# Kernel optimization log

Hardware: AMD Instinct MI355X
Metric: run time of the kernel (lower is better)

The kernel has to match this reference:

```python
import jax, jax.numpy as jnp
import numpy as np

K = 20        # num_neighbor
EPS = 1e-5    # BatchNorm eps


def setup_inputs() -> dict:
    key = jax.random.key(0)
    ks = jax.random.split(key, 3)
    B, C, N = 8, 64, 2048
    points = jax.random.normal(ks[0], (B, C, N), dtype=jnp.float32)
    # 1x1 conv weights (out_ch, in_ch); BN affine params
    W0 = jax.random.normal(ks[1], (64, 2 * C), dtype=jnp.float32) * 0.05
    W1 = jax.random.normal(ks[2], (64, 64), dtype=jnp.float32) * 0.05
    return {
        "points": points,
        "W0": W0, "gamma0": jnp.ones((64,), jnp.float32), "beta0": jnp.zeros((64,), jnp.float32),
        "W1": W1, "gamma1": jnp.ones((64,), jnp.float32), "beta1": jnp.zeros((64,), jnp.float32),
    }


def _knn_idx(points, k):
    # points: (B, C, N) -> indices of k nearest neighbors (B, N, k)
    inner = jnp.einsum('bcn,bcm->bnm', points, points)          # (B,N,N)
    sq = jnp.sum(points * points, axis=1)                        # (B,N)
    dist = sq[:, :, None] - 2.0 * inner + sq[:, None, :]         # squared L2
    _, idx = jax.lax.top_k(-dist, k)                             # (B,N,k)
    return idx


def _edge_features(points, idx):
    # points: (B,C,N), idx: (B,N,K) -> (B, 2C, N, K) = concat([x_i, x_j - x_i])
    B, C, N = points.shape
    neigh = jnp.take_along_axis(points[:, :, None, :],           # (B,C,1,N)
                                idx[:, None, :, :], axis=3)      # (B,C,N,K)
    center = jnp.broadcast_to(points[:, :, :, None], neigh.shape)
    return jnp.concatenate([center, neigh - center], axis=1)     # (B,2C,N,K)


def _conv_bn_relu(x, W, gamma, beta):
    # 1x1 conv (no bias) + BatchNorm2d (training-mode batch stats) + ReLU
    h = jnp.einsum('oi,bink->bonk', W, x)
    mean = jnp.mean(h, axis=(0, 2, 3), keepdims=True)
    var = jnp.var(h, axis=(0, 2, 3), keepdims=True)
    h = (h - mean) * jax.lax.rsqrt(var + EPS)
    h = h * gamma[None, :, None, None] + beta[None, :, None, None]
    return jax.nn.relu(h)


def reference(points, W0, gamma0, beta0, W1, gamma1, beta1):
    idx = _knn_idx(points, K)                  # (B,N,K)
    feat = _edge_features(points, idx)         # (B,2C,N,K)
    feat = _conv_bn_relu(feat, W0, gamma0, beta0)
    feat = _conv_bn_relu(feat, W1, gamma1, beta1)
    return jnp.max(feat, axis=3)               # (B, out_ch, N)
```

## Files before the change

### kernel.cpp

```cpp
#include <hip/hip_runtime.h>

#define NPTS 2048
#define NB 8
#define NC 64
#define KNN 20
#define NSLOT 16
#define NMERGE 28
#define EPS 1e-5f
#define MTOT 327680.0f

#define WS_U_BYTE    1024
#define WS_V_BYTE    4195328
#define WS_IDX_BYTE  8389632
#define WS_SQD_BYTE  9700352
#define WS_SQ32_BYTE 9831424
#define WS_HMIN_BYTE 9700352

__device__ __forceinline__ unsigned umax2(unsigned a, unsigned b) { return a > b ? a : b; }
__device__ __forceinline__ unsigned umin2(unsigned a, unsigned b) { return a < b ? a : b; }

__global__ __launch_bounds__(256) void k_prep(const float* __restrict__ pts,
                                              const float* __restrict__ W0,
                                              double* __restrict__ sqd,
                                              float* __restrict__ sq32,
                                              float* __restrict__ u,
                                              float* __restrict__ v) {
  const int b  = blockIdx.x >> 5;
  const int n0 = (blockIdx.x & 31) << 6;
  const int tid = threadIdx.x;
  __shared__ float WdT[64][64];
  __shared__ float WbT[64][64];
  __shared__ float xs[64][64];
  for (int i = tid; i < 4096; i += 256) {
    int o = i & 63, c = i >> 6;
    float wa = W0[o * 128 + c], wb = W0[o * 128 + 64 + c];
    WdT[c][o] = wa - wb;
    WbT[c][o] = wb;
  }
  {
    int pp = tid & 63, c0 = tid >> 6;
    for (int i = 0; i < 16; i++) {
      int c = c0 + 4 * i;
      xs[c][pp] = pts[(b * 64 + c) * NPTS + n0 + pp];
    }
  }
  __syncthreads();
  if (tid < 64) {
    double s = 0.0;
    for (int c = 0; c < 64; c++) { double x = (double)xs[c][tid]; s += x * x; }
    sqd[b * NPTS + n0 + tid] = s;
    sq32[b * NPTS + n0 + tid] = (float)s;
  }
  const int o = tid & 63, w = tid >> 6;
  float wd[64], wb[64];
#pragma unroll
  for (int c = 0; c < 64; c++) { wd[c] = WdT[c][o]; wb[c] = WbT[c][o]; }
  for (int i = 0; i < 16; i++) {
    int p = w + 4 * i;
    float ua = 0.f, va = 0.f;
#pragma unroll
    for (int c = 0; c < 64; c++) {
      float xc = xs[c][p];
      ua += wd[c] * xc;
      va += wb[c] * xc;
    }
    int gp = b * NPTS + n0 + p;
    u[gp * 64 + o] = ua;
    v[gp * 64 + o] = va;
  }
}

__global__ __launch_bounds__(64) void k_knn(const float* __restrict__ pts,
                                            const double* __restrict__ sqd,
                                            const float* __restrict__ sq32,
                                            int* __restrict__ idxout) {
  const int b  = blockIdx.x >> 9;
  const int n0 = (blockIdx.x & 511) << 2;
  const int lane = threadIdx.x;
  __shared__ __align__(16) float4 rows4[64];
  __shared__ __align__(16) float distS[1024];
  const float* pb = pts + b * 64 * NPTS;
  rows4[lane] = *(const float4*)(pb + lane * NPTS + n0);
  float sqr[4];
#pragma unroll
  for (int rr = 0; rr < 4; rr++) sqr[rr] = sq32[b * NPTS + n0 + rr];
  __syncthreads();

  unsigned slot[NSLOT];
#pragma unroll
  for (int j = 0; j < NSLOT; j++) slot[j] = 0xFFFFF800u | (unsigned)j;
  unsigned wmax = 0xFFFFF800u | (NSLOT - 1);
  const int r = lane >> 4, g = lane & 15;

  for (int t = 0; t < 8; t++) {
    const int mb = t * 256;
    float facc[16];
#pragma unroll
    for (int i = 0; i < 16; i++) facc[i] = 0.f;
    const float4 sqm = *(const float4*)(sq32 + b * NPTS + mb + 4 * lane);
#pragma unroll 8
    for (int c = 0; c < 64; c++) {
      float4 xm = *(const float4*)(pb + c * NPTS + mb + 4 * lane);
      float4 xr = rows4[c];
      facc[0]  += xr.x * xm.x; facc[1]  += xr.x * xm.y; facc[2]  += xr.x * xm.z; facc[3]  += xr.x * xm.w;
      facc[4]  += xr.y * xm.x; facc[5]  += xr.y * xm.y; facc[6]  += xr.y * xm.z; facc[7]  += xr.y * xm.w;
      facc[8]  += xr.z * xm.x; facc[9]  += xr.z * xm.y; facc[10] += xr.z * xm.z; facc[11] += xr.z * xm.w;
      facc[12] += xr.w * xm.x; facc[13] += xr.w * xm.y; facc[14] += xr.w * xm.z; facc[15] += xr.w * xm.w;
    }
#pragma unroll
    for (int rr = 0; rr < 4; rr++) {
      float4 dd;
      dd.x = sqr[rr] + sqm.x - 2.f * facc[rr * 4 + 0];
      dd.y = sqr[rr] + sqm.y - 2.f * facc[rr * 4 + 1];
      dd.z = sqr[rr] + sqm.z - 2.f * facc[rr * 4 + 2];
      dd.w = sqr[rr] + sqm.w - 2.f * facc[rr * 4 + 3];
      *(float4*)&distS[rr * 256 + (lane & 3) * 64 + (lane >> 2) * 4] = dd;
    }
    __syncthreads();
#pragma unroll
    for (int j4 = 0; j4 < 4; j4++) {
      float4 dv = *(const float4*)&distS[r * 256 + j4 * 64 + g * 4];
      float dq[4] = {dv.x, dv.y, dv.z, dv.w};
#pragma unroll
      for (int q = 0; q < 4; q++) {
        int m = mb + g * 16 + j4 * 4 + q;
        unsigned ub = __float_as_uint(dq[q]);
        ub ^= (ub >> 31) ? 0xFFFFFFFFu : 0x80000000u;
        unsigned key = (ub & 0xFFFFF800u) | (unsigned)m;
        if (key < wmax) {
#pragma unroll
          for (int j = 0; j < NSLOT; j++)
            slot[j] = (slot[j] == wmax) ? key : slot[j];
          unsigned t8[8];
#pragma unroll
          for (int j = 0; j < 8; j++) t8[j] = umax2(slot[2 * j], slot[2 * j + 1]);
          unsigned t4a = umax2(t8[0], t8[1]), t4b = umax2(t8[2], t8[3]);
          unsigned t4c = umax2(t8[4], t8[5]), t4d = umax2(t8[6], t8[7]);
          wmax = umax2(umax2(t4a, t4b), umax2(t4c, t4d));
        }
      }
    }
    __syncthreads();
  }

  unsigned mycand[2] = {0xFFFFFFFFu, 0xFFFFFFFFu};
  for (int p = 0; p < NMERGE; p++) {
    unsigned t8[8];
#pragma unroll
    for (int j = 0; j < 8; j++) t8[j] = umin2(slot[2 * j], slot[2 * j + 1]);
    unsigned t4a = umin2(t8[0], t8[1]), t4b = umin2(t8[2], t8[3]);
    unsigned t4c = umin2(t8[4], t8[5]), t4d = umin2(t8[6], t8[7]);
    unsigned gmin = umin2(umin2(t4a, t4b), umin2(t4c, t4d));
#pragma unroll
    for (int mk = 1; mk < 16; mk <<= 1) {
      unsigned o = __shfl_xor(gmin, mk, 16);
      gmin = umin2(gmin, o);
    }
#pragma unroll
    for (int j = 0; j < NSLOT; j++)
      if (slot[j] == gmin) slot[j] = 0xFFFFFFFFu;
    if ((p & 15) == g) mycand[p >> 4] = gmin;
  }

  const int nrow = n0 + r;
  const float* rowsF = (const float*)rows4;
  unsigned long long ekey[2];
#pragma unroll
  for (int s = 0; s < 2; s++) {
    ekey[s] = ~0ull;
    if (mycand[s] != 0xFFFFFFFFu) {
      const int m = (int)(mycand[s] & 2047u);
      const float* pc = pb + m;
      double a0 = 0.0, a1 = 0.0, a2 = 0.0, a3 = 0.0;
      for (int c = 0; c < 64; c += 4) {
        a0 += (double)rowsF[(c + 0) * 4 + r] * (double)pc[(c + 0) * NPTS];
        a1 += (double)rowsF[(c + 1) * 4 + r] * (double)pc[(c + 1) * NPTS];
        a2 += (double)rowsF[(c + 2) * 4 + r] * (double)pc[(c + 2) * NPTS];
        a3 += (double)rowsF[(c + 3) * 4 + r] * (double)pc[(c + 3) * NPTS];
      }
      double d = sqd[b * NPTS + nrow] + sqd[b * NPTS + m] - 2.0 * ((a0 + a1) + (a2 + a3));
      unsigned long long ub = (unsigned long long)__double_as_longlong(d);
      ub ^= (ub >> 63) ? 0xFFFFFFFFFFFFFFFFull : 0x8000000000000000ull;
      ekey[s] = (ub & ~2047ull) | (unsigned long long)(unsigned)m;
    }
  }

  const int row = b * NPTS + nrow;
  for (int p = 0; p < KNN; p++) {
    unsigned long long lmin = ekey[0] < ekey[1] ? ekey[0] : ekey[1];
#pragma unroll
    for (int mk = 1; mk < 16; mk <<= 1) {
      unsigned long long o = __shfl_xor(lmin, mk, 16);
      lmin = o < lmin ? o : lmin;
    }
    if (g == 0) idxout[row * KNN + p] = (int)(lmin & 2047ull);
    if (ekey[0] == lmin) ekey[0] = ~0ull;
    if (ekey[1] == lmin) ekey[1] = ~0ull;
  }
}

__global__ __launch_bounds__(256) void k_stats0(const float* __restrict__ u,
                                                const float* __restrict__ v,
                                                const int* __restrict__ idx,
                                                float* __restrict__ stats) {
  const int tid = threadIdx.x, o = tid & 63, w = tid >> 6;
  float s1 = 0.f, s2 = 0.f;
  const int r0 = blockIdx.x * 64;
  for (int i = 0; i < 16; i++) {
    int row = r0 + w + 4 * i;
    int b = row >> 11;
    float uo = u[row * 64 + o];
    const int* ip = idx + row * KNN;
    for (int k = 0; k < KNN; k++) {
      int j = ip[k];
      float h = uo + v[(b * NPTS + j) * 64 + o];
      s1 += h; s2 += h * h;
    }
  }
  __shared__ float red[2][256];
  red[0][tid] = s1; red[1][tid] = s2;
  __syncthreads();
  if (tid < 64) {
    float a  = red[0][tid] + red[0][tid + 64] + red[0][tid + 128] + red[0][tid + 192];
    float bb = red[1][tid] + red[1][tid + 64] + red[1][tid + 128] + red[1][tid + 192];
    atomicAdd(&stats[o], a);
    atomicAdd(&stats[64 + o], bb);
  }
}

__global__ __launch_bounds__(256) void k_mid(const float* __restrict__ u,
                                             const float* __restrict__ v,
                                             const int* __restrict__ idx,
                                             const float* __restrict__ W1,
                                             const float* __restrict__ g0,
                                             const float* __restrict__ b0,
                                             const float* __restrict__ stats0,
                                             float* __restrict__ stats1,
                                             float* __restrict__ hmax,
                                             float* __restrict__ hmin) {
  const int tid = threadIdx.x, o = tid & 63, w = tid >> 6;
  __shared__ float W1s[64][65];
  __shared__ float hbuf[4][4][64];
  for (int i = tid; i < 4096; i += 256) W1s[i >> 6][i & 63] = W1[i];
  __syncthreads();
  float mean = stats0[o] / MTOT;
  float var  = stats0[64 + o] / MTOT - mean * mean;
  float a0 = g0[o] * rsqrtf(var + EPS);
  float c0 = b0[o] - mean * a0;
  float w1r[64];
#pragma unroll
  for (int c = 0; c < 64; c++) w1r[c] = W1s[o][c];
  float s1 = 0.f, s2 = 0.f;
  const int r0 = blockIdx.x * 16 + w * 4;
  for (int rr = 0; rr < 4; rr++) {
    const int row = r0 + rr;
    const int b = row >> 11, n = row & 2047;
    const float uo = u[row * 64 + o];
    const int* ip = idx + row * KNN;
    float hmx = -1e30f, hmn = 1e30f;
    for (int kb = 0; kb < 5; kb++) {
#pragma unroll
      for (int kk = 0; kk < 4; kk++) {
        int j = ip[kb * 4 + kk];
        float h0 = uo + v[(b * NPTS + j) * 64 + o];
        hbuf[w][kk][o] = fmaxf(a0 * h0 + c0, 0.f);
      }
      __syncthreads();
#pragma unroll
      for (int kk = 0; kk < 4; kk++) {
        float h1 = 0.f;
#pragma unroll
        for (int c4 = 0; c4 < 16; c4++) {
          float4 hh = *(const float4*)&hbuf[w][kk][c4 * 4];
          h1 += w1r[c4 * 4 + 0] * hh.x + w1r[c4 * 4 + 1] * hh.y +
                w1r[c4 * 4 + 2] * hh.z + w1r[c4 * 4 + 3] * hh.w;
        }
        s1 += h1; s2 += h1 * h1;
        hmx = fmaxf(hmx, h1); hmn = fminf(hmn, h1);
      }
      __syncthreads();
    }
    hmax[(b * 64 + o) * NPTS + n] = hmx;
    hmin[(b * 64 + o) * NPTS + n] = hmn;
  }
  __shared__ float red[2][256];
  red[0][tid] = s1; red[1][tid] = s2;
  __syncthreads();
  if (tid < 64) {
    float a  = red[0][tid] + red[0][tid + 64] + red[0][tid + 128] + red[0][tid + 192];
    float bb = red[1][tid] + red[1][tid + 64] + red[1][tid + 128] + red[1][tid + 192];
    atomicAdd(&stats1[o], a);
    atomicAdd(&stats1[64 + o], bb);
  }
}

__global__ __launch_bounds__(256) void k_final(const float* __restrict__ hmaxO,
                                               const float* __restrict__ hmin,
                                               const float* __restrict__ stats1,
                                               const float* __restrict__ g1,
                                               const float* __restrict__ b1,
                                               float* __restrict__ out) {
  const int i = blockIdx.x * 256 + threadIdx.x;
  const int o = (i >> 11) & 63;
  float mean = stats1[o] / MTOT;
  float var  = stats1[64 + o] / MTOT - mean * mean;
  float a1 = g1[o] * rsqrtf(var + EPS);
  float c1 = b1[o] - mean * a1;
  float pick = (a1 >= 0.f) ? hmaxO[i] : hmin[i];
  out[i] = fmaxf(a1 * pick + c1, 0.f);
}

extern "C" void kernel_launch(void* const* d_in, const int* in_sizes, int n_in,
                              void* d_out, int out_size, void* d_ws, size_t ws_size,
                              hipStream_t stream) {
  const float* pts = (const float*)d_in[0];
  const float* W0  = (const float*)d_in[1];
  const float* g0  = (const float*)d_in[2];
  const float* b0  = (const float*)d_in[3];
  const float* W1  = (const float*)d_in[4];
  const float* g1  = (const float*)d_in[5];
  const float* b1  = (const float*)d_in[6];
  float* out = (float*)d_out;
  float* ws  = (float*)d_ws;

  float*  stats0 = ws;
  float*  stats1 = ws + 128;
  float*  u      = (float*)((char*)d_ws + WS_U_BYTE);
  float*  v      = (float*)((char*)d_ws + WS_V_BYTE);
  int*    idx    = (int*)((char*)d_ws + WS_IDX_BYTE);
  double* sqd    = (double*)((char*)d_ws + WS_SQD_BYTE);
  float*  sq32   = (float*)((char*)d_ws + WS_SQ32_BYTE);
  float*  hmin   = (float*)((char*)d_ws + WS_HMIN_BYTE);

  hipMemsetAsync(d_ws, 0, 1024, stream);
  k_prep  <<<256,  256, 0, stream>>>(pts, W0, sqd, sq32, u, v);
  k_knn   <<<4096,  64, 0, stream>>>(pts, sqd, sq32, idx);
  k_stats0<<<256,  256, 0, stream>>>(u, v, idx, stats0);
  k_mid   <<<1024, 256, 0, stream>>>(u, v, idx, W1, g0, b0, stats0, stats1, out, hmin);
  k_final <<<4096, 256, 0, stream>>>(out, hmin, stats1, g1, b1, out);
}
```

Before: 387.9 us.

## Split KNN work to two rows per wavefront, four wavefronts per block

The KNN kernel now handles two query rows per 64-lane wavefront instead of four, with 32 lanes per row, and packs four independent wavefronts into a 256-thread block. Block barriers are replaced by an LDS waitcnt fence because each wave only touches its own shared-memory slice. This doubles the total wavefronts and halves the per-lane register accumulators, aiming at more parallelism and occupancy for the selection phase. The cost is that the candidate points' global loads are now reused across only two rows rather than four, doubling redundant reads of the point matrix, and the fence-only synchronisation assumes single-wave lockstep.

```diff
diff --git a/kernel.cpp b/kernel.cpp
--- a/kernel.cpp
+++ b/kernel.cpp
@@ -15,6 +15,8 @@
 #define WS_SQD_BYTE  9700352
 #define WS_SQ32_BYTE 9831424
 #define WS_HMIN_BYTE 9700352
+
+#define LDS_FENCE() asm volatile("s_waitcnt lgkmcnt(0)" ::: "memory")
 
 __device__ __forceinline__ unsigned umax2(unsigned a, unsigned b) { return a > b ? a : b; }
 __device__ __forceinline__ unsigned umin2(unsigned a, unsigned b) { return a < b ? a : b; }
@@ -70,60 +72,59 @@
   }
 }
 
-__global__ __launch_bounds__(64) void k_knn(const float* __restrict__ pts,
-                                            const double* __restrict__ sqd,
-                                            const float* __restrict__ sq32,
-                                            int* __restrict__ idxout) {
-  const int b  = blockIdx.x >> 9;
-  const int n0 = (blockIdx.x & 511) << 2;
-  const int lane = threadIdx.x;
-  __shared__ __align__(16) float4 rows4[64];
-  __shared__ __align__(16) float distS[1024];
+__global__ __launch_bounds__(256, 8) void k_knn(const float* __restrict__ pts,
+                                                const double* __restrict__ sqd,
+                                                const float* __restrict__ sq32,
+                                                int* __restrict__ idxout) {
+  const int b   = blockIdx.x >> 8;
+  const int tid = threadIdx.x;
+  const int wv  = tid >> 6, lane = tid & 63;
+  const int n0  = ((blockIdx.x & 255) << 3) + (wv << 1);
+  __shared__ __align__(16) float2 rows2[4][64];
+  __shared__ __align__(16) float distS[4][512];
   const float* pb = pts + b * 64 * NPTS;
-  rows4[lane] = *(const float4*)(pb + lane * NPTS + n0);
-  float sqr[4];
-#pragma unroll
-  for (int rr = 0; rr < 4; rr++) sqr[rr] = sq32[b * NPTS + n0 + rr];
-  __syncthreads();
+  rows2[wv][lane] = *(const float2*)(pb + lane * NPTS + n0);
+  float sqr[2];
+#pragma unroll
+  for (int rr = 0; rr < 2; rr++) sqr[rr] = sq32[b * NPTS + n0 + rr];
+  LDS_FENCE();
 
   unsigned slot[NSLOT];
 #pragma unroll
   for (int j = 0; j < NSLOT; j++) slot[j] = 0xFFFFF800u | (unsigned)j;
   unsigned wmax = 0xFFFFF800u | (NSLOT - 1);
-  const int r = lane >> 4, g = lane & 15;
+  const int r = lane >> 5, g = lane & 31;
 
   for (int t = 0; t < 8; t++) {
     const int mb = t * 256;
-    float facc[16];
-#pragma unroll
-    for (int i = 0; i < 16; i++) facc[i] = 0.f;
+    float facc[8];
+#pragma unroll
+    for (int i = 0; i < 8; i++) facc[i] = 0.f;
     const float4 sqm = *(const float4*)(sq32 + b * NPTS + mb + 4 * lane);
 #pragma unroll 8
     for (int c = 0; c < 64; c++) {
       float4 xm = *(const float4*)(pb + c * NPTS + mb + 4 * lane);
-      float4 xr = rows4[c];
-      facc[0]  += xr.x * xm.x; facc[1]  += xr.x * xm.y; facc[2]  += xr.x * xm.z; facc[3]  += xr.x * xm.w;
-      facc[4]  += xr.y * xm.x; facc[5]  += xr.y * xm.y; facc[6]  += xr.y * xm.z; facc[7]  += xr.y * xm.w;
-      facc[8]  += xr.z * xm.x; facc[9]  += xr.z * xm.y; facc[10] += xr.z * xm.z; facc[11] += xr.z * xm.w;
-      facc[12] += xr.w * xm.x; facc[13] += xr.w * xm.y; facc[14] += xr.w * xm.z; facc[15] += xr.w * xm.w;
-    }
-#pragma unroll
-    for (int rr = 0; rr < 4; rr++) {
+      float2 xr = rows2[wv][c];
+      facc[0] += xr.x * xm.x; facc[1] += xr.x * xm.y; facc[2] += xr.x * xm.z; facc[3] += xr.x * xm.w;
+      facc[4] += xr.y * xm.x; facc[5] += xr.y * xm.y; facc[6] += xr.y * xm.z; facc[7] += xr.y * xm.w;
+    }
+#pragma unroll
+    for (int rr = 0; rr < 2; rr++) {
       float4 dd;
       dd.x = sqr[rr] + sqm.x - 2.f * facc[rr * 4 + 0];
       dd.y = sqr[rr] + sqm.y - 2.f * facc[rr * 4 + 1];
       dd.z = sqr[rr] + sqm.z - 2.f * facc[rr * 4 + 2];
       dd.w = sqr[rr] + sqm.w - 2.f * facc[rr * 4 + 3];
-      *(float4*)&distS[rr * 256 + (lane & 3) * 64 + (lane >> 2) * 4] = dd;
-    }
-    __syncthreads();
-#pragma unroll
-    for (int j4 = 0; j4 < 4; j4++) {
-      float4 dv = *(const float4*)&distS[r * 256 + j4 * 64 + g * 4];
+      *(float4*)&distS[wv][rr * 256 + (lane & 1) * 128 + (lane >> 1) * 4] = dd;
+    }
+    LDS_FENCE();
+#pragma unroll
+    for (int j4 = 0; j4 < 2; j4++) {
+      float4 dv = *(const float4*)&distS[wv][r * 256 + j4 * 128 + g * 4];
       float dq[4] = {dv.x, dv.y, dv.z, dv.w};
 #pragma unroll
       for (int q = 0; q < 4; q++) {
-        int m = mb + g * 16 + j4 * 4 + q;
+        int m = mb + g * 8 + j4 * 4 + q;
         unsigned ub = __float_as_uint(dq[q]);
         ub ^= (ub >> 31) ? 0xFFFFFFFFu : 0x80000000u;
         unsigned key = (ub & 0xFFFFF800u) | (unsigned)m;
@@ -140,10 +141,10 @@
         }
       }
     }
-    __syncthreads();
-  }
-
-  unsigned mycand[2] = {0xFFFFFFFFu, 0xFFFFFFFFu};
+    LDS_FENCE();
+  }
+
+  unsigned mycand = 0xFFFFFFFFu;
   for (int p = 0; p < NMERGE; p++) {
     unsigned t8[8];
 #pragma unroll
@@ -152,50 +153,45 @@
     unsigned t4c = umin2(t8[4], t8[5]), t4d = umin2(t8[6], t8[7]);
     unsigned gmin = umin2(umin2(t4a, t4b), umin2(t4c, t4d));
 #pragma unroll
-    for (int mk = 1; mk < 16; mk <<= 1) {
-      unsigned o = __shfl_xor(gmin, mk, 16);
+    for (int mk = 1; mk < 32; mk <<= 1) {
+      unsigned o = __shfl_xor(gmin, mk, 32);
       gmin = umin2(gmin, o);
     }
 #pragma unroll
     for (int j = 0; j < NSLOT; j++)
       if (slot[j] == gmin) slot[j] = 0xFFFFFFFFu;
-    if ((p & 15) == g) mycand[p >> 4] = gmin;
+    if (p == g) mycand = gmin;
   }
 
   const int nrow = n0 + r;
-  const float* rowsF = (const float*)rows4;
-  unsigned long long ekey[2];
-#pragma unroll
-  for (int s = 0; s < 2; s++) {
-    ekey[s] = ~0ull;
-    if (mycand[s] != 0xFFFFFFFFu) {
-      const int m = (int)(mycand[s] & 2047u);
-      const float* pc = pb + m;
-      double a0 = 0.0, a1 = 0.0, a2 = 0.0, a3 = 0.0;
-      for (int c = 0; c < 64; c += 4) {
-        a0 += (double)rowsF[(c + 0) * 4 + r] * (double)pc[(c + 0) * NPTS];
-        a1 += (double)rowsF[(c + 1) * 4 + r] * (double)pc[(c + 1) * NPTS];
-        a2 += (double)rowsF[(c + 2) * 4 + r] * (double)pc[(c + 2) * NPTS];
-        a3 += (double)rowsF[(c + 3) * 4 + r] * (double)pc[(c + 3) * NPTS];
-      }
-      double d = sqd[b * NPTS + nrow] + sqd[b * NPTS + m] - 2.0 * ((a0 + a1) + (a2 + a3));
-      unsigned long long ub = (unsigned long long)__double_as_longlong(d);
-      ub ^= (ub >> 63) ? 0xFFFFFFFFFFFFFFFFull : 0x8000000000000000ull;
-      ekey[s] = (ub & ~2047ull) | (unsigned long long)(unsigned)m;
-    }
+  const float* rowsF = (const float*)rows2[wv];
+  unsigned long long ekey = ~0ull;
+  if (mycand != 0xFFFFFFFFu) {
+    const int m = (int)(mycand & 2047u);
+    const float* pc = pb + m;
+    double a0 = 0.0, a1 = 0.0, a2 = 0.0, a3 = 0.0;
+    for (int c = 0; c < 64; c += 4) {
+      a0 += (double)rowsF[(c + 0) * 2 + r] * (double)pc[(c + 0) * NPTS];
+      a1 += (double)rowsF[(c + 1) * 2 + r] * (double)pc[(c + 1) * NPTS];
+      a2 += (double)rowsF[(c + 2) * 2 + r] * (double)pc[(c + 2) * NPTS];
+      a3 += (double)rowsF[(c + 3) * 2 + r] * (double)pc[(c + 3) * NPTS];
+    }
+    double d = sqd[b * NPTS + nrow] + sqd[b * NPTS + m] - 2.0 * ((a0 + a1) + (a2 + a3));
+    unsigned long long ub = (unsigned long long)__double_as_longlong(d);
+    ub ^= (ub >> 63) ? 0xFFFFFFFFFFFFFFFFull : 0x8000000000000000ull;
+    ekey = (ub & ~2047ull) | (unsigned long long)(unsigned)m;
   }
 
   const int row = b * NPTS + nrow;
   for (int p = 0; p < KNN; p++) {
-    unsigned long long lmin = ekey[0] < ekey[1] ? ekey[0] : ekey[1];
-#pragma unroll
-    for (int mk = 1; mk < 16; mk <<= 1) {
-      unsigned long long o = __shfl_xor(lmin, mk, 16);
+    unsigned long long lmin = ekey;
+#pragma unroll
+    for (int mk = 1; mk < 32; mk <<= 1) {
+      unsigned long long o = __shfl_xor(lmin, mk, 32);
       lmin = o < lmin ? o : lmin;
     }
     if (g == 0) idxout[row * KNN + p] = (int)(lmin & 2047ull);
-    if (ekey[0] == lmin) ekey[0] = ~0ull;
-    if (ekey[1] == lmin) ekey[1] = ~0ull;
+    if (ekey == lmin) ekey = ~0ull;
   }
 }
 
@@ -334,7 +330,7 @@
 
   hipMemsetAsync(d_ws, 0, 1024, stream);
   k_prep  <<<256,  256, 0, stream>>>(pts, W0, sqd, sq32, u, v);
-  k_knn   <<<4096,  64, 0, stream>>>(pts, sqd, sq32, idx);
+  k_knn   <<<2048, 256, 0, stream>>>(pts, sqd, sq32, idx);
   k_stats0<<<256,  256, 0, stream>>>(u, v, idx, stats0);
   k_mid   <<<1024, 256, 0, stream>>>(u, v, idx, W1, g0, b0, stats0, stats1, out, hmin);
   k_final <<<4096, 256, 0, stream>>>(out, hmin, stats1, g1, b1, out);
```

Measured after the change: 442.8 us. +14.2%, slower.

## Fuse layer-0 BN statistics into kNN kernel and drop block barriers in k_mid

Applied to the files above, without the earlier changes.

The separate k_stats0 kernel is removed. Its sum and sum-of-squares accumulation now runs at the end of k_knn, using neighbor indices kept in shared memory, and the atomics are spread over 8 replicated stat copies that k_mid sums. In k_mid the two __syncthreads per neighbor batch become plain LDS waitcnt fences, since each wave only touches its own hbuf slice. This saves a kernel launch, an idx re-read and barrier stalls, but adds many more global atomics (4096 blocks) and relies on wave-local LDS ordering being enough.

```diff
diff --git a/kernel.cpp b/kernel.cpp
--- a/kernel.cpp
+++ b/kernel.cpp
@@ -6,15 +6,18 @@
 #define KNN 20
 #define NSLOT 16
 #define NMERGE 28
+#define NCOPY 8
 #define EPS 1e-5f
 #define MTOT 327680.0f
 
-#define WS_U_BYTE    1024
-#define WS_V_BYTE    4195328
-#define WS_IDX_BYTE  8389632
-#define WS_SQD_BYTE  9700352
-#define WS_SQ32_BYTE 9831424
-#define WS_HMIN_BYTE 9700352
+#define WS_U_BYTE    5120
+#define WS_V_BYTE    4199424
+#define WS_IDX_BYTE  8393728
+#define WS_SQD_BYTE  9704448
+#define WS_SQ32_BYTE 9835520
+#define WS_HMIN_BYTE 9704448
+
+#define LDS_FENCE() asm volatile("s_waitcnt lgkmcnt(0)" ::: "memory")
 
 __device__ __forceinline__ unsigned umax2(unsigned a, unsigned b) { return a > b ? a : b; }
 __device__ __forceinline__ unsigned umin2(unsigned a, unsigned b) { return a < b ? a : b; }
@@ -73,12 +76,16 @@
 __global__ __launch_bounds__(64) void k_knn(const float* __restrict__ pts,
                                             const double* __restrict__ sqd,
                                             const float* __restrict__ sq32,
-                                            int* __restrict__ idxout) {
+                                            const float* __restrict__ u,
+                                            const float* __restrict__ v,
+                                            int* __restrict__ idxout,
+                                            float* __restrict__ stats0c) {
   const int b  = blockIdx.x >> 9;
   const int n0 = (blockIdx.x & 511) << 2;
   const int lane = threadIdx.x;
   __shared__ __align__(16) float4 rows4[64];
   __shared__ __align__(16) float distS[1024];
+  __shared__ int widxS[4][KNN];
   const float* pb = pts + b * 64 * NPTS;
   rows4[lane] = *(const float4*)(pb + lane * NPTS + n0);
   float sqr[4];
@@ -193,39 +200,30 @@
       unsigned long long o = __shfl_xor(lmin, mk, 16);
       lmin = o < lmin ? o : lmin;
     }
-    if (g == 0) idxout[row * KNN + p] = (int)(lmin & 2047ull);
+    if (g == 0) {
+      idxout[row * KNN + p] = (int)(lmin & 2047ull);
+      widxS[r][p] = (int)(lmin & 2047ull);
+    }
     if (ekey[0] == lmin) ekey[0] = ~0ull;
     if (ekey[1] == lmin) ekey[1] = ~0ull;
   }
-}
-
-__global__ __launch_bounds__(256) void k_stats0(const float* __restrict__ u,
-                                                const float* __restrict__ v,
-                                                const int* __restrict__ idx,
-                                                float* __restrict__ stats) {
-  const int tid = threadIdx.x, o = tid & 63, w = tid >> 6;
+
+  __syncthreads();
+  const int ch = lane;
   float s1 = 0.f, s2 = 0.f;
-  const int r0 = blockIdx.x * 64;
-  for (int i = 0; i < 16; i++) {
-    int row = r0 + w + 4 * i;
-    int b = row >> 11;
-    float uo = u[row * 64 + o];
-    const int* ip = idx + row * KNN;
+#pragma unroll
+  for (int rr = 0; rr < 4; rr++) {
+    const int grow = b * NPTS + n0 + rr;
+    const float uo = u[grow * 64 + ch];
     for (int k = 0; k < KNN; k++) {
-      int j = ip[k];
-      float h = uo + v[(b * NPTS + j) * 64 + o];
+      int j = widxS[rr][k];
+      float h = uo + v[(b * NPTS + j) * 64 + ch];
       s1 += h; s2 += h * h;
     }
   }
-  __shared__ float red[2][256];
-  red[0][tid] = s1; red[1][tid] = s2;
-  __syncthreads();
-  if (tid < 64) {
-    float a  = red[0][tid] + red[0][tid + 64] + red[0][tid + 128] + red[0][tid + 192];
-    float bb = red[1][tid] + red[1][tid + 64] + red[1][tid + 128] + red[1][tid + 192];
-    atomicAdd(&stats[o], a);
-    atomicAdd(&stats[64 + o], bb);
-  }
+  float* sc = stats0c + (blockIdx.x & (NCOPY - 1)) * 128;
+  atomicAdd(&sc[ch], s1);
+  atomicAdd(&sc[64 + ch], s2);
 }
 
 __global__ __launch_bounds__(256) void k_mid(const float* __restrict__ u,
@@ -234,7 +232,7 @@
                                              const float* __restrict__ W1,
                                              const float* __restrict__ g0,
                                              const float* __restrict__ b0,
-                                             const float* __restrict__ stats0,
+                                             const float* __restrict__ stats0c,
                                              float* __restrict__ stats1,
                                              float* __restrict__ hmax,
                                              float* __restrict__ hmin) {
@@ -243,8 +241,14 @@
   __shared__ float hbuf[4][4][64];
   for (int i = tid; i < 4096; i += 256) W1s[i >> 6][i & 63] = W1[i];
   __syncthreads();
-  float mean = stats0[o] / MTOT;
-  float var  = stats0[64 + o] / MTOT - mean * mean;
+  float ms = 0.f, qs = 0.f;
+#pragma unroll
+  for (int cc = 0; cc < NCOPY; cc++) {
+    ms += stats0c[cc * 128 + o];
+    qs += stats0c[cc * 128 + 64 + o];
+  }
+  float mean = ms / MTOT;
+  float var  = qs / MTOT - mean * mean;
   float a0 = g0[o] * rsqrtf(var + EPS);
   float c0 = b0[o] - mean * a0;
   float w1r[64];
@@ -265,7 +269,7 @@
         float h0 = uo + v[(b * NPTS + j) * 64 + o];
         hbuf[w][kk][o] = fmaxf(a0 * h0 + c0, 0.f);
       }
-      __syncthreads();
+      LDS_FENCE();
 #pragma unroll
       for (int kk = 0; kk < 4; kk++) {
         float h1 = 0.f;
@@ -278,7 +282,7 @@
         s1 += h1; s2 += h1 * h1;
         hmx = fmaxf(hmx, h1); hmn = fminf(hmn, h1);
       }
-      __syncthreads();
+      LDS_FENCE();
     }
     hmax[(b * 64 + o) * NPTS + n] = hmx;
     hmin[(b * 64 + o) * NPTS + n] = hmn;
@@ -323,8 +327,8 @@
   float* out = (float*)d_out;
   float* ws  = (float*)d_ws;
 
-  float*  stats0 = ws;
-  float*  stats1 = ws + 128;
+  float*  stats0c = ws;
+  float*  stats1  = ws + 1024;
   float*  u      = (float*)((char*)d_ws + WS_U_BYTE);
   float*  v      = (float*)((char*)d_ws + WS_V_BYTE);
   int*    idx    = (int*)((char*)d_ws + WS_IDX_BYTE);
@@ -332,10 +336,9 @@
   float*  sq32   = (float*)((char*)d_ws + WS_SQ32_BYTE);
   float*  hmin   = (float*)((char*)d_ws + WS_HMIN_BYTE);
 
-  hipMemsetAsync(d_ws, 0, 1024, stream);
-  k_prep  <<<256,  256, 0, stream>>>(pts, W0, sqd, sq32, u, v);
-  k_knn   <<<4096,  64, 0, stream>>>(pts, sqd, sq32, idx);
-  k_stats0<<<256,  256, 0, stream>>>(u, v, idx, stats0);
-  k_mid   <<<1024, 256, 0, stream>>>(u, v, idx, W1, g0, b0, stats0, stats1, out, hmin);
-  k_final <<<4096, 256, 0, stream>>>(out, hmin, stats1, g1, b1, out);
-}
+  hipMemsetAsync(d_ws, 0, 4608, stream);
+  k_prep <<<256,  256, 0, stream>>>(pts, W0, sqd, sq32, u, v);
+  k_knn  <<<4096,  64, 0, stream>>>(pts, sqd, sq32, u, v, idx, stats0c);
+  k_mid  <<<1024, 256, 0, stream>>>(u, v, idx, W1, g0, b0, stats0c, stats1, out, hmin);
+  k_final<<<4096, 256, 0, stream>>>(out, hmin, stats1, g1, b1, out);
+}
```

Result: faster. 373.5 us (-3.7%).
